# Kernel tuning notes

Measured on AMD Instinct MI355X. Metric: run time of the kernel, lower is better.

The kernel has to match this reference:

```python
import jax, jax.numpy as jnp
import numpy as np

N, E, C, L, NG = 50000, 600000, 128, 7, 512
EPS = 1e-7


def layer_norm(z, g, b):
    mu = z.mean(-1, keepdims=True)
    var = ((z - mu) ** 2).mean(-1, keepdims=True)
    return (z - mu) * jax.lax.rsqrt(var + 1e-5) * g + b


def setup_inputs() -> dict:
    key = jax.random.key(0)
    ks = jax.random.split(key, 16)
    inp = {
        'x': jax.random.randint(ks[0], (N, 9), 0, 64, dtype=jnp.int32),
        'edge_index': jax.random.randint(ks[1], (2, E), 0, N, dtype=jnp.int32),
        'edge_attr': jax.random.randint(ks[2], (E, 3), 0, 8, dtype=jnp.int32),
        'batch': jnp.sort(jax.random.randint(ks[3], (N,), 0, NG, dtype=jnp.int32)),
        'atom_emb': jax.random.normal(ks[4], (9, 64, C), jnp.float32) * 0.1,
        'bond_emb': jax.random.normal(ks[5], (3, 8, C), jnp.float32) * 0.1,
        'vn_emb': jnp.zeros((1, C), jnp.float32),
        'conv_W1': jax.random.normal(ks[6], (L, C, 2 * C), jnp.float32) / np.sqrt(C),
        'conv_b1': jnp.zeros((L, 2 * C), jnp.float32),
        'conv_g1': jnp.ones((L, 2 * C), jnp.float32),
        'conv_bb1': jnp.zeros((L, 2 * C), jnp.float32),
        'conv_W2': jax.random.normal(ks[7], (L, 2 * C, C), jnp.float32) / np.sqrt(2 * C),
        'conv_b2': jnp.zeros((L, C), jnp.float32),
        'norm_g': jnp.ones((L, C), jnp.float32),
        'norm_b': jnp.zeros((L, C), jnp.float32),
        'vn_W1': jax.random.normal(ks[8], (L - 1, C, C), jnp.float32) / np.sqrt(C),
        'vn_b1': jnp.zeros((L - 1, C), jnp.float32),
        'vn_g': jnp.ones((L - 1, C), jnp.float32),
        'vn_bb': jnp.zeros((L - 1, C), jnp.float32),
        'vn_W2': jax.random.normal(ks[9], (L - 1, C, C), jnp.float32) / np.sqrt(C),
        'vn_b2': jnp.zeros((L - 1, C), jnp.float32),
    }
    return inp


def reference(x, edge_index, edge_attr, batch, atom_emb, bond_emb, vn_emb,
              conv_W1, conv_b1, conv_g1, conv_bb1, conv_W2, conv_b2,
              norm_g, norm_b, vn_W1, vn_b1, vn_g, vn_bb, vn_W2, vn_b2):
    src, dst = edge_index[0], edge_index[1]

    # AtomEncoder: sum of per-feature embeddings -> [N, C]
    h = atom_emb[jnp.arange(9), x].sum(axis=1)
    # BondEncoder (conv_encode_edge=False) -> [E, C]
    edge_emb = bond_emb[jnp.arange(3), edge_attr].sum(axis=1)

    # virtual node embedding (one per graph)
    vn = jnp.broadcast_to(vn_emb[0], (NG, C))
    h = h + vn[batch]

    def gen_conv(l, hx):
        # GENConv: msg = relu(x_j + e) + eps; softmax aggregation (t=1); MLP(x+m)
        msg = jax.nn.relu(hx[src] + edge_emb) + EPS                      # [E, C]
        mx = jax.ops.segment_max(msg, dst, num_segments=N)               # [N, C]
        e = jnp.exp(msg - mx[dst])
        den = jax.ops.segment_sum(e, dst, num_segments=N)
        m = jax.ops.segment_sum(msg * (e / (den[dst] + 1e-16)), dst, num_segments=N)
        z = hx + m
        z = jax.nn.relu(layer_norm(z @ conv_W1[l] + conv_b1[l], conv_g1[l], conv_bb1[l]))
        return z @ conv_W2[l] + conv_b2[l]

    # res+ block: Conv -> [Norm -> ReLU -> (VN update) -> Conv + res]*
    h = gen_conv(0, h)
    for l in range(1, L):
        h2 = jax.nn.relu(layer_norm(h, norm_g[l - 1], norm_b[l - 1]))
        vtmp = jax.ops.segment_sum(h2, batch, num_segments=NG) + vn
        v = jax.nn.relu(layer_norm(vtmp @ vn_W1[l - 1] + vn_b1[l - 1], vn_g[l - 1], vn_bb[l - 1]))
        vn = v @ vn_W2[l - 1] + vn_b2[l - 1]
        h2 = h2 + vn[batch]
        h = gen_conv(l, h2) + h
    h = layer_norm(h, norm_g[L - 1], norm_b[L - 1])

    # global_add_pool -> [NG, C]
    return jax.ops.segment_sum(h, batch, num_segments=NG)
```

## Files before the change

kernel.cpp:

```cpp
#include <hip/hip_runtime.h>
#include <hip/hip_bf16.h>
#include <stdint.h>

#define N_NODES 50000
#define N_EDGES 600000
#define CH 128
#define NLAYERS 7
#define NGRAPHS 512

typedef __hip_bfloat16 bf16;
using bf16x8 = __attribute__((ext_vector_type(8))) __bf16;
using f32x4  = __attribute__((ext_vector_type(4))) float;
using u32x4  = __attribute__((ext_vector_type(4))) uint32_t;

static __device__ __forceinline__ float b2f(bf16 v){ return __bfloat162float(v); }

static __device__ __forceinline__ void bar_lds(){
  asm volatile("s_waitcnt lgkmcnt(0)" ::: "memory");
  __builtin_amdgcn_sched_barrier(0);
  __builtin_amdgcn_s_barrier();
}

__global__ void k_detect(const uint32_t* __restrict__ g, int* __restrict__ flag){
  if (threadIdx.x == 0 && blockIdx.x == 0) flag[0] = (g[0] == 0x3F803F80u) ? 1 : 0;
}

struct Segs { const void* src[12]; float* dst[12]; int n[12]; };

__global__ void k_cvt_all(const int* __restrict__ flag, Segs S){
  int f = flag[0];
  int seg = blockIdx.y;
  int n = S.n[seg];
  const void* src = S.src[seg];
  float* dst = S.dst[seg];
  for (int i = blockIdx.x*blockDim.x + threadIdx.x; i < n; i += gridDim.x*blockDim.x)
    dst[i] = f ? b2f(((const bf16*)src)[i]) : ((const float*)src)[i];
}

__global__ void k_transpose_all(const int* __restrict__ flag,
    const void* W1, const void* W2, const void* vW1, const void* vW2,
    bf16* W1p, bf16* W2T, bf16* vW1p, bf16* vW2T){
  int f = flag[0];
  const int T0 = NLAYERS*128*256, T1 = NLAYERS*256*128;
  const int T2 = (NLAYERS-1)*128*128;
  int total = T0+T1+2*T2;
  for (int i = blockIdx.x*blockDim.x + threadIdx.x; i < total; i += gridDim.x*blockDim.x){
    float v;
    if (i < T0){
      int idx = i; int l = idx/(128*256); int rem = idx - l*128*256; int k = rem >> 8; int n = rem & 255;
      v = f ? b2f(((const bf16*)W1)[idx]) : ((const float*)W1)[idx];
      W1p[(size_t)l*256*128 + n*128 + (k ^ ((n&7)<<3))] = __float2bfloat16(v);
    } else if (i < T0+T1){
      int idx = i-T0; int l = idx/(256*128); int rem = idx - l*256*128; int k = rem >> 7; int n = rem & 127;
      v = f ? b2f(((const bf16*)W2)[idx]) : ((const float*)W2)[idx];
      W2T[(size_t)l*128*256 + n*256 + k] = __float2bfloat16(v);
    } else if (i < T0+T1+T2){
      int idx = i-T0-T1; int l = idx/(128*128); int rem = idx - l*128*128; int k = rem >> 7; int n = rem & 127;
      v = f ? b2f(((const bf16*)vW1)[idx]) : ((const float*)vW1)[idx];
      vW1p[(size_t)l*128*128 + n*128 + (k ^ ((n&7)<<3))] = __float2bfloat16(v);
    } else {
      int idx = i-T0-T1-T2; int l = idx/(128*128); int rem = idx - l*128*128; int k = rem >> 7; int n = rem & 127;
      v = f ? b2f(((const bf16*)vW2)[idx]) : ((const float*)vW2)[idx];
      vW2T[(size_t)l*128*128 + n*128 + k] = __float2bfloat16(v);
    }
  }
}

__global__ void k_bondC(const int* __restrict__ flag, const void* __restrict__ bond,
                        float* __restrict__ bondC){
  int f = flag[0];
  int i = blockIdx.x*blockDim.x + threadIdx.x;
  if (i >= 512*128) return;
  int idx = i >> 7, c = i & 127;
  int a0 = idx & 7, a1 = (idx>>3) & 7, a2 = (idx>>6) & 7;
  auto g = [&](int e)->float{ return f ? b2f(((const bf16*)bond)[e]) : ((const float*)bond)[e]; };
  bondC[i] = g((0*8+a0)*128 + c) + g((1*8+a1)*128 + c) + g((2*8+a2)*128 + c);
}

__global__ void k_zero_i32(int* p, int n){
  for (int i = blockIdx.x*blockDim.x + threadIdx.x; i < n; i += gridDim.x*blockDim.x) p[i] = 0;
}

__global__ void k_hist(const int* __restrict__ keys, int* __restrict__ counts, int n){
  for (int i = blockIdx.x*blockDim.x + threadIdx.x; i < n; i += gridDim.x*blockDim.x)
    atomicAdd(&counts[keys[i]], 1);
}

__global__ __launch_bounds__(256) void k_scanA(const int* __restrict__ in, int* __restrict__ out,
                                               int* __restrict__ bsums, int n){
  __shared__ int lds[256];
  int t = threadIdx.x;
  int base = blockIdx.x * 1024;
  int v[4]; int s = 0;
  #pragma unroll
  for (int i=0;i<4;i++){ int idx = base + t*4 + i; int x = (idx<n)? in[idx] : 0; v[i]=x; s+=x; }
  lds[t] = s; __syncthreads();
  for (int off=1; off<256; off<<=1){
    int x = (t>=off)? lds[t-off] : 0;
    __syncthreads();
    lds[t] += x;
    __syncthreads();
  }
  int p = lds[t] - s;
  #pragma unroll
  for (int i=0;i<4;i++){ int idx = base + t*4 + i; if (idx<n) out[idx] = p; p += v[i]; }
  if (t==255) bsums[blockIdx.x] = lds[255];
}

__global__ __launch_bounds__(256) void k_scanB(int* bsums, int nblk){
  __shared__ int lds[256];
  int t = threadIdx.x;
  int v = (t<nblk)? bsums[t] : 0;
  lds[t] = v; __syncthreads();
  for (int off=1; off<256; off<<=1){
    int x = (t>=off)? lds[t-off] : 0;
    __syncthreads();
    lds[t] += x;
    __syncthreads();
  }
  if (t<nblk) bsums[t] = lds[t] - v;
}

__global__ void k_scanC(int* out, const int* bsums, int n){
  for (int i = blockIdx.x*blockDim.x + threadIdx.x; i < n; i += gridDim.x*blockDim.x)
    out[i] += bsums[i >> 10];
}

__global__ void k_scatter(const int* __restrict__ ei, const int* __restrict__ ea,
                          const int* __restrict__ row_ptr, int* __restrict__ fill,
                          uint32_t* __restrict__ csr){
  for (int e = blockIdx.x*blockDim.x + threadIdx.x; e < N_EDGES; e += gridDim.x*blockDim.x){
    int src = ei[e];
    int dst = ei[N_EDGES + e];
    int pos = row_ptr[dst] + atomicAdd(&fill[dst], 1);
    uint32_t a0 = (uint32_t)ea[e*3+0], a1 = (uint32_t)ea[e*3+1], a2 = (uint32_t)ea[e*3+2];
    csr[pos] = (uint32_t)src | ((a0 | (a1<<3) | (a2<<6)) << 16);
  }
}

__global__ void k_gptr(const int* __restrict__ batch, int* __restrict__ gptr){
  int i = blockIdx.x*blockDim.x + threadIdx.x;
  if (i >= N_NODES) return;
  int b = batch[i];
  if (i == 0){ for (int g=0; g<=b; ++g) gptr[g] = 0; }
  else { int bp = batch[i-1]; for (int g=bp+1; g<=b; ++g) gptr[g] = i; }
  if (i == N_NODES-1){ for (int g=b+1; g<=NGRAPHS; ++g) gptr[g] = N_NODES; }
}

__global__ __launch_bounds__(128) void k_atom_encode(const int* __restrict__ x,
    const float* __restrict__ atom_emb, const float* __restrict__ vn_emb,
    uint32_t* __restrict__ hxb){
  int n = blockIdx.x; int c = threadIdx.x;
  float s = vn_emb[c];
  #pragma unroll
  for (int f=0; f<9; ++f){
    int xv = x[n*9+f];
    s += atom_emb[(f*64 + xv)*CH + c];
  }
  float o = __shfl_xor(s, 1);
  if ((c & 1) == 0){
    __hip_bfloat162 p; p.x = __float2bfloat16(s); p.y = __float2bfloat16(o);
    hxb[n*64 + (c>>1)] = *reinterpret_cast<uint32_t*>(&p);
  }
}

__global__ void k_vn_init(const float* __restrict__ vn_emb, float* __restrict__ vn){
  for (int i = blockIdx.x*blockDim.x + threadIdx.x; i < NGRAPHS*CH; i += gridDim.x*blockDim.x)
    vn[i] = vn_emb[i & (CH-1)];
}

__global__ __launch_bounds__(64) void k_aggregate(const uint32_t* __restrict__ hxb,
     const uint32_t* __restrict__ csr, const int* __restrict__ row_ptr,
     const float* __restrict__ bondC, uint32_t* __restrict__ z){
  int n = blockIdx.x; int t = threadIdx.x;
  int s0 = row_ptr[n], s1 = row_ptr[n+1];
  float sa=0.f, sb=0.f, wa=0.f, wb=0.f;
  int i = s0;
  for (; i+4 <= s1; i += 4){
    uint32_t u0=csr[i], u1=csr[i+1], u2=csr[i+2], u3=csr[i+3];
    uint32_t h0 = hxb[(size_t)(u0 & 0xFFFFu)*64 + t];
    uint32_t h1 = hxb[(size_t)(u1 & 0xFFFFu)*64 + t];
    uint32_t h2 = hxb[(size_t)(u2 & 0xFFFFu)*64 + t];
    uint32_t h3 = hxb[(size_t)(u3 & 0xFFFFu)*64 + t];
    float2 c0 = *reinterpret_cast<const float2*>(bondC + (size_t)(u0 >> 16)*128 + 2*t);
    float2 c1 = *reinterpret_cast<const float2*>(bondC + (size_t)(u1 >> 16)*128 + 2*t);
    float2 c2 = *reinterpret_cast<const float2*>(bondC + (size_t)(u2 >> 16)*128 + 2*t);
    float2 c3 = *reinterpret_cast<const float2*>(bondC + (size_t)(u3 >> 16)*128 + 2*t);
    #define EDGE(hp, bc) { \
      float va = __uint_as_float(hp << 16) + bc.x; \
      float vb = __uint_as_float(hp & 0xFFFF0000u) + bc.y; \
      va = fmaxf(va, 0.f) + 1e-7f; vb = fmaxf(vb, 0.f) + 1e-7f; \
      float pa = __expf(va - 10.f), pb = __expf(vb - 10.f); \
      sa += pa; wa += pa*va; sb += pb; wb += pb*vb; }
    EDGE(h0, c0) EDGE(h1, c1) EDGE(h2, c2) EDGE(h3, c3)
  }
  for (; i < s1; ++i){
    uint32_t u = csr[i];
    uint32_t hp = hxb[(size_t)(u & 0xFFFFu)*64 + t];
    float2 bc = *reinterpret_cast<const float2*>(bondC + (size_t)(u >> 16)*128 + 2*t);
    EDGE(hp, bc)
    #undef EDGE
  }
  uint32_t own = hxb[(size_t)n*64 + t];
  float za = __uint_as_float(own << 16)         + wa/(sa + 1e-16f);
  float zb = __uint_as_float(own & 0xFFFF0000u) + wb/(sb + 1e-16f);
  __hip_bfloat162 p; p.x = __float2bfloat16(za); p.y = __float2bfloat16(zb);
  z[(size_t)n*64 + (t ^ ((n&7)<<2))] = *reinterpret_cast<uint32_t*>(&p);
}

template<int K, int N1, int N2, bool VNIN>
__global__ __launch_bounds__(512, 2) void k_mlp7(const bf16* __restrict__ A,
    const float* __restrict__ Af32,
    const bf16* __restrict__ W1s,
    const float* __restrict__ b1, const float* __restrict__ g1, const float* __restrict__ bb1,
    const bf16* __restrict__ W2T,
    const float* __restrict__ b2,
    const float* __restrict__ lng, const float* __restrict__ lnb,
    const float* __restrict__ residual, float* __restrict__ out,
    float* __restrict__ hxout, int relu2, int M, int NT)
{
  constexpr int KK1 = K/32;
  constexpr int WC  = N1/4;
  constexpr int JC  = WC/16;
  constexpr int KK2 = N1/32;
  __shared__ __align__(16) bf16 W1L[N1*K];
  __shared__ __align__(16) bf16 AL[2][64*K];
  __shared__ __align__(16) bf16 zt[64*N1];
  __shared__ float lnp[64][4][2];
  __shared__ float lnv[64][2];

  const int tid = threadIdx.x;
  const int wid = tid >> 6, lane = tid & 63;
  const int wr = wid >> 2, wc = wid & 3;
  const int rlo = lane & 15, hi = lane >> 4, khi = hi*8;

  {
    constexpr int NC_ = (N1*K*2)/1024/8;
    #pragma unroll
    for (int c=0;c<NC_;++c){
      int cc = c*8 + wid;
      __builtin_amdgcn_global_load_lds((const uint32_t*)((const char*)W1s + cc*1024 + lane*16),
                                       (uint32_t*)((char*)W1L + cc*1024), 16, 0, 0);
    }
  }

  float b1v[JC], gv[JC], bbv[JC];
  #pragma unroll
  for (int jc=0;jc<JC;++jc){
    int col = wc*WC + jc*16 + rlo;
    b1v[jc] = b1[col]; gv[jc] = g1[col]; bbv[jc] = bb1[col];
  }
  float bv2[2] = { b2[wc*32 + rlo], b2[wc*32 + 16 + rlo] };
  float lngv[2] = {0.f,0.f}, lnbv[2] = {0.f,0.f};
  if (hxout){
    lngv[0] = lng[wc*32 + rlo];      lnbv[0] = lnb[wc*32 + rlo];
    lngv[1] = lng[wc*32 + 16 + rlo]; lnbv[1] = lnb[wc*32 + 16 + rlo];
  }
  u32x4 b2raw[2][KK2];
  #pragma unroll
  for (int ct=0;ct<2;++ct){
    const bf16* wp = W2T + (size_t)(wc*32 + ct*16 + rlo)*N1 + khi;
    #pragma unroll
    for (int kk=0;kk<KK2;++kk){
      b2raw[ct][kk] = *reinterpret_cast<const u32x4*>(wp + kk*32);
      asm volatile("" : "+v"(b2raw[ct][kk]));
    }
  }

  auto stageA = [&](int nb, int tile){
    if constexpr (!VNIN){
      const char* src = (const char*)A + (size_t)tile*(64*K*2);
      constexpr int NCA = (64*K*2)/1024/8;
      #pragma unroll
      for (int c=0;c<NCA;++c){
        int cc = c*8 + wid;
        __builtin_amdgcn_global_load_lds((const uint32_t*)(src + cc*1024 + lane*16),
                                         (uint32_t*)((char*)&AL[nb][0] + cc*1024), 16, 0, 0);
      }
    } else {
      int base = tile*64;
      #pragma unroll
      for (int e=0;e<(64*K/4)/512;++e){
        int idx = tid + e*512;
        int row = idx >> 5;
        int k4  = (idx & 31)*4;
        float4 v = *reinterpret_cast<const float4*>(Af32 + (size_t)(base+row)*K + k4);
        int s = (row&7)<<3;
        bf16* d = &AL[nb][row*K + (k4 ^ s)];
        d[0]=__float2bfloat16(v.x); d[1]=__float2bfloat16(v.y);
        d[2]=__float2bfloat16(v.z); d[3]=__float2bfloat16(v.w);
      }
    }
  };

  int t = blockIdx.x, buf = 0;
  stageA(0, t);
  __syncthreads();

  while (true){
    int tn = t + (int)gridDim.x;

    f32x4 acc1[2][JC];
    #pragma unroll
    for (int rt=0;rt<2;++rt)
      #pragma unroll
      for (int jc=0;jc<JC;++jc) acc1[rt][jc] = {0.f,0.f,0.f,0.f};
    #pragma unroll
    for (int kk=0;kk<KK1;++kk){
      bf16x8 af[2], bw[JC];
      #pragma unroll
      for (int rt=0;rt<2;++rt){
        int lr = wr*32 + rt*16 + rlo;
        af[rt] = *reinterpret_cast<const bf16x8*>(&AL[buf][lr*K + ((kk*32 + khi) ^ ((lr&7)<<3))]);
      }
      #pragma unroll
      for (int jc=0;jc<JC;++jc){
        int n = wc*WC + jc*16 + rlo;
        bw[jc] = *reinterpret_cast<const bf16x8*>(&W1L[n*K + ((kk*32 + khi) ^ ((n&7)<<3))]);
      }
      #pragma unroll
      for (int rt=0;rt<2;++rt)
        #pragma unroll
        for (int jc=0;jc<JC;++jc)
          acc1[rt][jc] = __builtin_amdgcn_mfma_f32_16x16x32_bf16(af[rt], bw[jc], acc1[rt][jc], 0,0,0);
    }

    if (tn < NT) stageA(buf^1, tn);
    float resv[2][2][4];
    if (residual){
      #pragma unroll
      for (int rt=0;rt<2;++rt)
        #pragma unroll
        for (int r=0;r<4;++r){
          int grow = t*64 + wr*32 + rt*16 + hi*4 + r; if (grow >= M) grow = M-1;
          #pragma unroll
          for (int ct=0;ct<2;++ct)
            resv[rt][ct][r] = residual[(size_t)grow*N2 + wc*32 + ct*16 + rlo];
        }
    }
    __builtin_amdgcn_sched_barrier(0);

    float p[2][4], q[2][4];
    #pragma unroll
    for (int rt=0;rt<2;++rt)
      #pragma unroll
      for (int r=0;r<4;++r){ p[rt][r]=0.f; q[rt][r]=0.f; }
    #pragma unroll
    for (int jc=0;jc<JC;++jc)
      #pragma unroll
      for (int rt=0;rt<2;++rt)
        #pragma unroll
        for (int r=0;r<4;++r){
          float v = acc1[rt][jc][r] + b1v[jc]; acc1[rt][jc][r] = v;
          p[rt][r] += v; q[rt][r] += v*v;
        }
    #pragma unroll
    for (int rt=0;rt<2;++rt)
      #pragma unroll
      for (int r=0;r<4;++r){
        float pv = p[rt][r], qv = q[rt][r];
        #pragma unroll
        for (int off=1; off<16; off<<=1){ pv += __shfl_xor(pv, off); qv += __shfl_xor(qv, off); }
        if (rlo == 0){
          int row = wr*32 + rt*16 + hi*4 + r;
          lnp[row][wc][0] = pv; lnp[row][wc][1] = qv;
        }
      }
    bar_lds();
    if (tid < 64){
      float P=0.f, Q=0.f;
      #pragma unroll
      for (int w=0;w<4;++w){ P += lnp[tid][w][0]; Q += lnp[tid][w][1]; }
      float mu = P*(1.f/N1);
      lnv[tid][0] = mu;
      lnv[tid][1] = rsqrtf(Q*(1.f/N1) - mu*mu + 1e-5f);
    }
    bar_lds();

    #pragma unroll
    for (int rt=0;rt<2;++rt)
      #pragma unroll
      for (int r=0;r<4;++r){
        int row = wr*32 + rt*16 + hi*4 + r;
        float mu = lnv[row][0], rs = lnv[row][1];
        #pragma unroll
        for (int jc=0;jc<JC;++jc){
          int col = wc*WC + jc*16 + rlo;
          float y = (acc1[rt][jc][r]-mu)*rs*gv[jc] + bbv[jc];
          zt[row*N1 + (col ^ ((row&7)<<3))] = __float2bfloat16(fmaxf(y, 0.f));
        }
      }
    bar_lds();

    f32x4 acc2[2][2];
    #pragma unroll
    for (int rt=0;rt<2;++rt)
      #pragma unroll
      for (int ct=0;ct<2;++ct) acc2[rt][ct] = {0.f,0.f,0.f,0.f};
    #pragma unroll
    for (int kk=0;kk<KK2;++kk){
      bf16x8 a2[2];
      #pragma unroll
      for (int rt=0;rt<2;++rt){
        int row = wr*32 + rt*16 + rlo;
        a2[rt] = *reinterpret_cast<const bf16x8*>(&zt[row*N1 + ((kk*32 + khi) ^ ((row&7)<<3))]);
      }
      #pragma unroll
      for (int rt=0;rt<2;++rt)
        #pragma unroll
        for (int ct=0;ct<2;++ct){
          bf16x8 bb;
          __builtin_memcpy(&bb, &b2raw[ct][kk], 16);
          acc2[rt][ct] = __builtin_amdgcn_mfma_f32_16x16x32_bf16(a2[rt], bb, acc2[rt][ct], 0,0,0);
        }
    }

    float vmat[2][2][4];
    #pragma unroll
    for (int rt=0;rt<2;++rt)
      #pragma unroll
      for (int ct=0;ct<2;++ct)
        #pragma unroll
        for (int r=0;r<4;++r){
          float v = acc2[rt][ct][r] + bv2[ct];
          if (residual) v += resv[rt][ct][r];
          vmat[rt][ct][r] = v;
          int grow = t*64 + wr*32 + rt*16 + hi*4 + r;
          if (grow < M) out[(size_t)grow*N2 + wc*32 + ct*16 + rlo] = v;
        }

    if (hxout){
      #pragma unroll
      for (int rt=0;rt<2;++rt)
        #pragma unroll
        for (int r=0;r<4;++r){
          float pv = vmat[rt][0][r] + vmat[rt][1][r];
          float qv = vmat[rt][0][r]*vmat[rt][0][r] + vmat[rt][1][r]*vmat[rt][1][r];
          #pragma unroll
          for (int off=1; off<16; off<<=1){ pv += __shfl_xor(pv, off); qv += __shfl_xor(qv, off); }
          if (rlo == 0){
            int row = wr*32 + rt*16 + hi*4 + r;
            lnp[row][wc][0] = pv; lnp[row][wc][1] = qv;
          }
        }
      bar_lds();
      if (tid < 64){
        float P=0.f, Q=0.f;
        #pragma unroll
        for (int w=0;w<4;++w){ P += lnp[tid][w][0]; Q += lnp[tid][w][1]; }
        float mu = P*(1.f/N2);
        lnv[tid][0] = mu;
        lnv[tid][1] = rsqrtf(Q*(1.f/N2) - mu*mu + 1e-5f);
      }
      bar_lds();
      #pragma unroll
      for (int rt=0;rt<2;++rt)
        #pragma unroll
        for (int r=0;r<4;++r){
          int row = wr*32 + rt*16 + hi*4 + r;
          float mu = lnv[row][0], rs = lnv[row][1];
          int grow = t*64 + row;
          if (grow < M){
            #pragma unroll
            for (int ct=0;ct<2;++ct){
              float y = (vmat[rt][ct][r]-mu)*rs*lngv[ct] + lnbv[ct];
              if (relu2) y = fmaxf(y, 0.f);
              hxout[(size_t)grow*N2 + wc*32 + ct*16 + rlo] = y;
            }
          }
        }
    }

    if (tn >= NT) break;
    t = tn; buf ^= 1;
    __syncthreads();
  }
}

__global__ void k_vncopy(const float* __restrict__ vn, float* __restrict__ vnacc){
  int i = blockIdx.x*blockDim.x + threadIdx.x;
  if (i < NGRAPHS*CH) vnacc[i] = vn[i];
}

#define SEGC 128
__global__ __launch_bounds__(128) void k_segsum2(const float* __restrict__ hx,
    const int* __restrict__ batch, float* __restrict__ vnacc){
  int c = threadIdx.x;
  int n0 = blockIdx.x*SEGC;
  int n1 = n0 + SEGC; if (n1 > N_NODES) n1 = N_NODES;
  if (n0 >= N_NODES) return;
  int cur = batch[n0];
  float s = 0.f;
  for (int n = n0; n < n1; ++n){
    int b = batch[n];
    if (b != cur){ atomicAdd(&vnacc[cur*CH + c], s); s = 0.f; cur = b; }
    s += hx[(size_t)n*CH + c];
  }
  atomicAdd(&vnacc[cur*CH + c], s);
}

__global__ void k_add_vn(const float* __restrict__ hx, const float* __restrict__ vn,
                         const int* __restrict__ batch, uint32_t* __restrict__ hxb){
  for (int i = blockIdx.x*blockDim.x + threadIdx.x; i < N_NODES*64; i += gridDim.x*blockDim.x){
    int n = i >> 6; int t = i & 63;
    float2 hv = *reinterpret_cast<const float2*>(hx + (size_t)n*CH + 2*t);
    float2 vv = *reinterpret_cast<const float2*>(vn + (size_t)batch[n]*CH + 2*t);
    __hip_bfloat162 p; p.x = __float2bfloat16(hv.x+vv.x); p.y = __float2bfloat16(hv.y+vv.y);
    hxb[i] = *reinterpret_cast<uint32_t*>(&p);
  }
}

__global__ __launch_bounds__(128) void k_pool(const float* __restrict__ hx,
    const int* __restrict__ gptr, const int* __restrict__ flag, void* __restrict__ out){
  int g = blockIdx.x; int c = threadIdx.x;
  float s = 0.f;
  for (int n = gptr[g]; n < gptr[g+1]; ++n) s += hx[(size_t)n*CH + c];
  if (flag[0]) ((bf16*)out)[g*CH+c] = __float2bfloat16(s);
  else         ((float*)out)[g*CH+c] = s;
}

extern "C" void kernel_launch(void* const* d_in, const int* in_sizes, int n_in,
                              void* d_out, int out_size, void* d_ws, size_t ws_size,
                              hipStream_t stream)
{
  const int*  x     = (const int*) d_in[0];
  const int*  ei    = (const int*) d_in[1];
  const int*  ea    = (const int*) d_in[2];
  const int*  batch = (const int*) d_in[3];
  const void* atom_emb = d_in[4];
  const void* bond_emb = d_in[5];
  const void* vn_emb   = d_in[6];
  const void* conv_W1  = d_in[7];
  const void* conv_b1  = d_in[8];
  const void* conv_g1  = d_in[9];
  const void* conv_bb1 = d_in[10];
  const void* conv_W2  = d_in[11];
  const void* conv_b2  = d_in[12];
  const void* norm_g   = d_in[13];
  const void* norm_b   = d_in[14];
  const void* vn_W1    = d_in[15];
  const void* vn_b1    = d_in[16];
  const void* vn_g     = d_in[17];
  const void* vn_bb    = d_in[18];
  const void* vn_W2    = d_in[19];
  const void* vn_b2    = d_in[20];

  char* wsb = (char*)d_ws;
  size_t off = 0;
  auto alloc = [&](size_t bytes)->char*{ char* p = wsb + off; off += (bytes + 255) & ~(size_t)255; return p; };
  const int ZROWS = 50048;
  float*    h     = (float*)   alloc(sizeof(float)*N_NODES*CH);
  float*    hx    = (float*)   alloc(sizeof(float)*N_NODES*CH);
  uint32_t* hxb   = (uint32_t*)alloc(sizeof(uint32_t)*N_NODES*64);
  uint32_t* z     = (uint32_t*)alloc(sizeof(uint32_t)*ZROWS*64);
  float*    vn    = (float*)   alloc(sizeof(float)*NGRAPHS*CH);
  float*    vnacc = (float*)   alloc(sizeof(float)*NGRAPHS*CH);
  bf16*     W1Tp  = (bf16*)    alloc(sizeof(bf16)*NLAYERS*256*128);
  bf16*     W2T   = (bf16*)    alloc(sizeof(bf16)*NLAYERS*128*256);
  bf16*     vW1Tp = (bf16*)    alloc(sizeof(bf16)*(NLAYERS-1)*128*128);
  bf16*     vW2T  = (bf16*)    alloc(sizeof(bf16)*(NLAYERS-1)*128*128);
  int* row_ptr = (int*)alloc(sizeof(int)*(N_NODES+1));
  int* counts  = (int*)alloc(sizeof(int)*(N_NODES+1));
  uint32_t* csr = (uint32_t*)alloc(sizeof(uint32_t)*N_EDGES);
  int* gptr    = (int*)alloc(sizeof(int)*(NGRAPHS+1));
  int* bsums   = (int*)alloc(sizeof(int)*256);
  int* flag    = (int*)alloc(sizeof(int)*64);
  float* atomF = (float*)alloc(sizeof(float)*9*64*CH);
  float* bondC = (float*)alloc(sizeof(float)*512*CH);
  float* vnEF  = (float*)alloc(sizeof(float)*CH);
  float* b1F   = (float*)alloc(sizeof(float)*NLAYERS*2*CH);
  float* g1F   = (float*)alloc(sizeof(float)*NLAYERS*2*CH);
  float* bb1F  = (float*)alloc(sizeof(float)*NLAYERS*2*CH);
  float* b2F   = (float*)alloc(sizeof(float)*NLAYERS*CH);
  float* ngF   = (float*)alloc(sizeof(float)*NLAYERS*CH);
  float* nbF   = (float*)alloc(sizeof(float)*NLAYERS*CH);
  float* vb1F  = (float*)alloc(sizeof(float)*(NLAYERS-1)*CH);
  float* vgF   = (float*)alloc(sizeof(float)*(NLAYERS-1)*CH);
  float* vbbF  = (float*)alloc(sizeof(float)*(NLAYERS-1)*CH);
  float* vb2F  = (float*)alloc(sizeof(float)*(NLAYERS-1)*CH);

  k_detect<<<1, 64, 0, stream>>>((const uint32_t*)norm_g, flag);
  Segs S;
  int si = 0;
  auto seg = [&](const void* s_, float* d_, int n_){ S.src[si]=s_; S.dst[si]=d_; S.n[si]=n_; ++si; };
  seg(atom_emb, atomF, 9*64*CH);
  seg(vn_emb,   vnEF,  CH);
  seg(conv_b1,  b1F,  NLAYERS*2*CH);
  seg(conv_g1,  g1F,  NLAYERS*2*CH);
  seg(conv_bb1, bb1F, NLAYERS*2*CH);
  seg(conv_b2,  b2F,  NLAYERS*CH);
  seg(norm_g,   ngF,  NLAYERS*CH);
  seg(norm_b,   nbF,  NLAYERS*CH);
  seg(vn_b1,    vb1F, (NLAYERS-1)*CH);
  seg(vn_g,     vgF,  (NLAYERS-1)*CH);
  seg(vn_bb,    vbbF, (NLAYERS-1)*CH);
  seg(vn_b2,    vb2F, (NLAYERS-1)*CH);
  k_cvt_all<<<dim3(72, 12), 256, 0, stream>>>(flag, S);
  k_transpose_all<<<640, 256, 0, stream>>>(flag, conv_W1, conv_W2, vn_W1, vn_W2,
                                           W1Tp, W2T, vW1Tp, vW2T);
  k_bondC<<<256, 256, 0, stream>>>(flag, bond_emb, bondC);

  k_zero_i32<<<64, 256, 0, stream>>>(counts, N_NODES+1);
  k_hist<<<512, 256, 0, stream>>>(ei + N_EDGES, counts, N_EDGES);
  int nblkE = (N_NODES+1 + 1023)/1024;
  k_scanA<<<nblkE, 256, 0, stream>>>(counts, row_ptr, bsums, N_NODES+1);
  k_scanB<<<1, 256, 0, stream>>>(bsums, nblkE);
  k_scanC<<<64, 256, 0, stream>>>(row_ptr, bsums, N_NODES+1);
  k_zero_i32<<<64, 256, 0, stream>>>(counts, N_NODES+1);
  k_scatter<<<512, 256, 0, stream>>>(ei, ea, row_ptr, counts, csr);
  k_gptr<<<(N_NODES+255)/256, 256, 0, stream>>>(batch, gptr);

  k_atom_encode<<<N_NODES, 128, 0, stream>>>(x, atomF, vnEF, hxb);
  k_vn_init<<<64, 256, 0, stream>>>(vnEF, vn);

  const int NT_CONV = (N_NODES + 63)/64;
  const int NT_VN   = NGRAPHS/64;

  for (int l = 0; l < NLAYERS; ++l){
    if (l > 0){
      k_vncopy<<<(NGRAPHS*CH+255)/256, 256, 0, stream>>>(vn, vnacc);
      k_segsum2<<<(N_NODES+SEGC-1)/SEGC, 128, 0, stream>>>(hx, batch, vnacc);
      k_mlp7<128,128,128,true><<<NT_VN, 512, 0, stream>>>(nullptr, vnacc,
          vW1Tp + (size_t)(l-1)*128*128, vb1F + (l-1)*CH, vgF + (l-1)*CH, vbbF + (l-1)*CH,
          vW2T + (size_t)(l-1)*128*128, vb2F + (l-1)*CH,
          nullptr, nullptr, nullptr, vn, nullptr, 0, NGRAPHS, NT_VN);
      k_add_vn<<<1024, 256, 0, stream>>>(hx, vn, batch, hxb);
    }
    k_aggregate<<<N_NODES, 64, 0, stream>>>(hxb, csr, row_ptr, bondC, z);
    k_mlp7<128,256,128,false><<<256, 512, 0, stream>>>((const bf16*)z, nullptr,
        W1Tp + (size_t)l*256*128, b1F + l*2*CH, g1F + l*2*CH, bb1F + l*2*CH,
        W2T + (size_t)l*128*256, b2F + l*CH,
        ngF + l*CH, nbF + l*CH,
        (l==0)? nullptr : h, h, hx, (l < NLAYERS-1) ? 1 : 0, N_NODES, NT_CONV);
  }
  k_pool<<<NGRAPHS, 128, 0, stream>>>(hx, gptr, flag, d_out);
}
```

Baseline: 965.8 us.

## Store residual, normalized activations and bond table in bf16; remap aggregate block order

Switches the residual stream h and the normalized activation hx from fp32 to bf16 storage. The MLP kernel gains a BF16IO template path, and segsum, add_vn and pool now read bf16. The bond combination table is also packed as bf16 pairs, and k_aggregate interleaves node indices across blocks in groups of eight. This halves memory traffic for the per-layer activation reads and writes, at the cost of accumulating the residual in bf16 across seven layers, which risks accuracy drift.

```diff
diff --git a/kernel.cpp b/kernel.cpp
--- a/kernel.cpp
+++ b/kernel.cpp
@@ -67,14 +67,18 @@
 }
 
 __global__ void k_bondC(const int* __restrict__ flag, const void* __restrict__ bond,
-                        float* __restrict__ bondC){
+                        uint32_t* __restrict__ bondC){
+  int i = blockIdx.x*blockDim.x + threadIdx.x;
+  if (i >= 512*64) return;
   int f = flag[0];
-  int i = blockIdx.x*blockDim.x + threadIdx.x;
-  if (i >= 512*128) return;
-  int idx = i >> 7, c = i & 127;
+  int idx = i >> 6, t = i & 63;
   int a0 = idx & 7, a1 = (idx>>3) & 7, a2 = (idx>>6) & 7;
   auto g = [&](int e)->float{ return f ? b2f(((const bf16*)bond)[e]) : ((const float*)bond)[e]; };
-  bondC[i] = g((0*8+a0)*128 + c) + g((1*8+a1)*128 + c) + g((2*8+a2)*128 + c);
+  int c0 = 2*t, c1 = 2*t+1;
+  float s0 = g((0*8+a0)*128 + c0) + g((1*8+a1)*128 + c0) + g((2*8+a2)*128 + c0);
+  float s1 = g((0*8+a0)*128 + c1) + g((1*8+a1)*128 + c1) + g((2*8+a2)*128 + c1);
+  __hip_bfloat162 p; p.x = __float2bfloat16(s0); p.y = __float2bfloat16(s1);
+  bondC[i] = *reinterpret_cast<uint32_t*>(&p);
 }
 
 __global__ void k_zero_i32(int* p, int n){
@@ -171,8 +175,9 @@
 
 __global__ __launch_bounds__(64) void k_aggregate(const uint32_t* __restrict__ hxb,
      const uint32_t* __restrict__ csr, const int* __restrict__ row_ptr,
-     const float* __restrict__ bondC, uint32_t* __restrict__ z){
-  int n = blockIdx.x; int t = threadIdx.x;
+     const uint32_t* __restrict__ bondC, uint32_t* __restrict__ z){
+  int n = (blockIdx.x & 7)*(N_NODES/8) + (blockIdx.x >> 3);
+  int t = threadIdx.x;
   int s0 = row_ptr[n], s1 = row_ptr[n+1];
   float sa=0.f, sb=0.f, wa=0.f, wb=0.f;
   int i = s0;
@@ -182,13 +187,13 @@
     uint32_t h1 = hxb[(size_t)(u1 & 0xFFFFu)*64 + t];
     uint32_t h2 = hxb[(size_t)(u2 & 0xFFFFu)*64 + t];
     uint32_t h3 = hxb[(size_t)(u3 & 0xFFFFu)*64 + t];
-    float2 c0 = *reinterpret_cast<const float2*>(bondC + (size_t)(u0 >> 16)*128 + 2*t);
-    float2 c1 = *reinterpret_cast<const float2*>(bondC + (size_t)(u1 >> 16)*128 + 2*t);
-    float2 c2 = *reinterpret_cast<const float2*>(bondC + (size_t)(u2 >> 16)*128 + 2*t);
-    float2 c3 = *reinterpret_cast<const float2*>(bondC + (size_t)(u3 >> 16)*128 + 2*t);
+    uint32_t c0 = bondC[(size_t)(u0 >> 16)*64 + t];
+    uint32_t c1 = bondC[(size_t)(u1 >> 16)*64 + t];
+    uint32_t c2 = bondC[(size_t)(u2 >> 16)*64 + t];
+    uint32_t c3 = bondC[(size_t)(u3 >> 16)*64 + t];
     #define EDGE(hp, bc) { \
-      float va = __uint_as_float(hp << 16) + bc.x; \
-      float vb = __uint_as_float(hp & 0xFFFF0000u) + bc.y; \
+      float va = __uint_as_float(hp << 16) + __uint_as_float(bc << 16); \
+      float vb = __uint_as_float(hp & 0xFFFF0000u) + __uint_as_float(bc & 0xFFFF0000u); \
       va = fmaxf(va, 0.f) + 1e-7f; vb = fmaxf(vb, 0.f) + 1e-7f; \
       float pa = __expf(va - 10.f), pb = __expf(vb - 10.f); \
       sa += pa; wa += pa*va; sb += pb; wb += pb*vb; }
@@ -197,7 +202,7 @@
   for (; i < s1; ++i){
     uint32_t u = csr[i];
     uint32_t hp = hxb[(size_t)(u & 0xFFFFu)*64 + t];
-    float2 bc = *reinterpret_cast<const float2*>(bondC + (size_t)(u >> 16)*128 + 2*t);
+    uint32_t bc = bondC[(size_t)(u >> 16)*64 + t];
     EDGE(hp, bc)
     #undef EDGE
   }
@@ -208,16 +213,16 @@
   z[(size_t)n*64 + (t ^ ((n&7)<<2))] = *reinterpret_cast<uint32_t*>(&p);
 }
 
-template<int K, int N1, int N2, bool VNIN>
-__global__ __launch_bounds__(512, 2) void k_mlp7(const bf16* __restrict__ A,
+template<int K, int N1, int N2, bool VNIN, bool BF16IO>
+__global__ __launch_bounds__(512, 2) void k_mlp12(const bf16* __restrict__ A,
     const float* __restrict__ Af32,
     const bf16* __restrict__ W1s,
     const float* __restrict__ b1, const float* __restrict__ g1, const float* __restrict__ bb1,
     const bf16* __restrict__ W2T,
     const float* __restrict__ b2,
     const float* __restrict__ lng, const float* __restrict__ lnb,
-    const float* __restrict__ residual, float* __restrict__ out,
-    float* __restrict__ hxout, int relu2, int M, int NT)
+    const void* __restrict__ residual, void* __restrict__ out,
+    bf16* __restrict__ hxn, int relu2, int M, int NT)
 {
   constexpr int KK1 = K/32;
   constexpr int WC  = N1/4;
@@ -252,7 +257,7 @@
   }
   float bv2[2] = { b2[wc*32 + rlo], b2[wc*32 + 16 + rlo] };
   float lngv[2] = {0.f,0.f}, lnbv[2] = {0.f,0.f};
-  if (hxout){
+  if (hxn){
     lngv[0] = lng[wc*32 + rlo];      lnbv[0] = lnb[wc*32 + rlo];
     lngv[1] = lng[wc*32 + 16 + rlo]; lnbv[1] = lnb[wc*32 + 16 + rlo];
   }
@@ -334,8 +339,11 @@
         for (int r=0;r<4;++r){
           int grow = t*64 + wr*32 + rt*16 + hi*4 + r; if (grow >= M) grow = M-1;
           #pragma unroll
-          for (int ct=0;ct<2;++ct)
-            resv[rt][ct][r] = residual[(size_t)grow*N2 + wc*32 + ct*16 + rlo];
+          for (int ct=0;ct<2;++ct){
+            size_t off = (size_t)grow*N2 + wc*32 + ct*16 + rlo;
+            resv[rt][ct][r] = BF16IO ? b2f(((const bf16*)residual)[off])
+                                     : ((const float*)residual)[off];
+          }
         }
     }
     __builtin_amdgcn_sched_barrier(0);
@@ -426,10 +434,14 @@
           if (residual) v += resv[rt][ct][r];
           vmat[rt][ct][r] = v;
           int grow = t*64 + wr*32 + rt*16 + hi*4 + r;
-          if (grow < M) out[(size_t)grow*N2 + wc*32 + ct*16 + rlo] = v;
-        }
-
-    if (hxout){
+          if (grow < M){
+            size_t off = (size_t)grow*N2 + wc*32 + ct*16 + rlo;
+            if (BF16IO) ((bf16*)out)[off] = __float2bfloat16(v);
+            else        ((float*)out)[off] = v;
+          }
+        }
+
+    if (hxn){
       #pragma unroll
       for (int rt=0;rt<2;++rt)
         #pragma unroll
@@ -465,7 +477,7 @@
             for (int ct=0;ct<2;++ct){
               float y = (vmat[rt][ct][r]-mu)*rs*lngv[ct] + lnbv[ct];
               if (relu2) y = fmaxf(y, 0.f);
-              hxout[(size_t)grow*N2 + wc*32 + ct*16 + rlo] = y;
+              hxn[(size_t)grow*N2 + wc*32 + ct*16 + rlo] = __float2bfloat16(y);
             }
           }
         }
@@ -483,7 +495,7 @@
 }
 
 #define SEGC 128
-__global__ __launch_bounds__(128) void k_segsum2(const float* __restrict__ hx,
+__global__ __launch_bounds__(128) void k_segsum2(const bf16* __restrict__ hxn,
     const int* __restrict__ batch, float* __restrict__ vnacc){
   int c = threadIdx.x;
   int n0 = blockIdx.x*SEGC;
@@ -494,27 +506,29 @@
   for (int n = n0; n < n1; ++n){
     int b = batch[n];
     if (b != cur){ atomicAdd(&vnacc[cur*CH + c], s); s = 0.f; cur = b; }
-    s += hx[(size_t)n*CH + c];
+    s += b2f(hxn[(size_t)n*CH + c]);
   }
   atomicAdd(&vnacc[cur*CH + c], s);
 }
 
-__global__ void k_add_vn(const float* __restrict__ hx, const float* __restrict__ vn,
+__global__ void k_add_vn(const uint32_t* __restrict__ hxn, const float* __restrict__ vn,
                          const int* __restrict__ batch, uint32_t* __restrict__ hxb){
   for (int i = blockIdx.x*blockDim.x + threadIdx.x; i < N_NODES*64; i += gridDim.x*blockDim.x){
     int n = i >> 6; int t = i & 63;
-    float2 hv = *reinterpret_cast<const float2*>(hx + (size_t)n*CH + 2*t);
+    uint32_t hp = hxn[i];
     float2 vv = *reinterpret_cast<const float2*>(vn + (size_t)batch[n]*CH + 2*t);
-    __hip_bfloat162 p; p.x = __float2bfloat16(hv.x+vv.x); p.y = __float2bfloat16(hv.y+vv.y);
+    float za = __uint_as_float(hp << 16)         + vv.x;
+    float zb = __uint_as_float(hp & 0xFFFF0000u) + vv.y;
+    __hip_bfloat162 p; p.x = __float2bfloat16(za); p.y = __float2bfloat16(zb);
     hxb[i] = *reinterpret_cast<uint32_t*>(&p);
   }
 }
 
-__global__ __launch_bounds__(128) void k_pool(const float* __restrict__ hx,
+__global__ __launch_bounds__(128) void k_pool(const bf16* __restrict__ hxn,
     const int* __restrict__ gptr, const int* __restrict__ flag, void* __restrict__ out){
   int g = blockIdx.x; int c = threadIdx.x;
   float s = 0.f;
-  for (int n = gptr[g]; n < gptr[g+1]; ++n) s += hx[(size_t)n*CH + c];
+  for (int n = gptr[g]; n < gptr[g+1]; ++n) s += b2f(hxn[(size_t)n*CH + c]);
   if (flag[0]) ((bf16*)out)[g*CH+c] = __float2bfloat16(s);
   else         ((float*)out)[g*CH+c] = s;
 }
@@ -549,8 +563,8 @@
   size_t off = 0;
   auto alloc = [&](size_t bytes)->char*{ char* p = wsb + off; off += (bytes + 255) & ~(size_t)255; return p; };
   const int ZROWS = 50048;
-  float*    h     = (float*)   alloc(sizeof(float)*N_NODES*CH);
-  float*    hx    = (float*)   alloc(sizeof(float)*N_NODES*CH);
+  uint32_t* hb    = (uint32_t*)alloc(sizeof(uint32_t)*ZROWS*64);
+  uint32_t* hxn   = (uint32_t*)alloc(sizeof(uint32_t)*ZROWS*64);
   uint32_t* hxb   = (uint32_t*)alloc(sizeof(uint32_t)*N_NODES*64);
   uint32_t* z     = (uint32_t*)alloc(sizeof(uint32_t)*ZROWS*64);
   float*    vn    = (float*)   alloc(sizeof(float)*NGRAPHS*CH);
@@ -566,7 +580,7 @@
   int* bsums   = (int*)alloc(sizeof(int)*256);
   int* flag    = (int*)alloc(sizeof(int)*64);
   float* atomF = (float*)alloc(sizeof(float)*9*64*CH);
-  float* bondC = (float*)alloc(sizeof(float)*512*CH);
+  uint32_t* bondC = (uint32_t*)alloc(sizeof(uint32_t)*512*64);
   float* vnEF  = (float*)alloc(sizeof(float)*CH);
   float* b1F   = (float*)alloc(sizeof(float)*NLAYERS*2*CH);
   float* g1F   = (float*)alloc(sizeof(float)*NLAYERS*2*CH);
@@ -598,7 +612,7 @@
   k_cvt_all<<<dim3(72, 12), 256, 0, stream>>>(flag, S);
   k_transpose_all<<<640, 256, 0, stream>>>(flag, conv_W1, conv_W2, vn_W1, vn_W2,
                                            W1Tp, W2T, vW1Tp, vW2T);
-  k_bondC<<<256, 256, 0, stream>>>(flag, bond_emb, bondC);
+  k_bondC<<<128, 256, 0, stream>>>(flag, bond_emb, bondC);
 
   k_zero_i32<<<64, 256, 0, stream>>>(counts, N_NODES+1);
   k_hist<<<512, 256, 0, stream>>>(ei + N_EDGES, counts, N_EDGES);
@@ -619,19 +633,20 @@
   for (int l = 0; l < NLAYERS; ++l){
     if (l > 0){
       k_vncopy<<<(NGRAPHS*CH+255)/256, 256, 0, stream>>>(vn, vnacc);
-      k_segsum2<<<(N_NODES+SEGC-1)/SEGC, 128, 0, stream>>>(hx, batch, vnacc);
-      k_mlp7<128,128,128,true><<<NT_VN, 512, 0, stream>>>(nullptr, vnacc,
+      k_segsum2<<<(N_NODES+SEGC-1)/SEGC, 128, 0, stream>>>((const bf16*)hxn, batch, vnacc);
+      k_mlp12<128,128,128,true,false><<<NT_VN, 512, 0, stream>>>(nullptr, vnacc,
           vW1Tp + (size_t)(l-1)*128*128, vb1F + (l-1)*CH, vgF + (l-1)*CH, vbbF + (l-1)*CH,
           vW2T + (size_t)(l-1)*128*128, vb2F + (l-1)*CH,
           nullptr, nullptr, nullptr, vn, nullptr, 0, NGRAPHS, NT_VN);
-      k_add_vn<<<1024, 256, 0, stream>>>(hx, vn, batch, hxb);
+      k_add_vn<<<1024, 256, 0, stream>>>(hxn, vn, batch, hxb);
     }
     k_aggregate<<<N_NODES, 64, 0, stream>>>(hxb, csr, row_ptr, bondC, z);
-    k_mlp7<128,256,128,false><<<256, 512, 0, stream>>>((const bf16*)z, nullptr,
+    k_mlp12<128,256,128,false,true><<<256, 512, 0, stream>>>((const bf16*)z, nullptr,
         W1Tp + (size_t)l*256*128, b1F + l*2*CH, g1F + l*2*CH, bb1F + l*2*CH,
         W2T + (size_t)l*128*256, b2F + l*CH,
         ngF + l*CH, nbF + l*CH,
-        (l==0)? nullptr : h, h, hx, (l < NLAYERS-1) ? 1 : 0, N_NODES, NT_CONV);
-  }
-  k_pool<<<NGRAPHS, 128, 0, stream>>>(hx, gptr, flag, d_out);
-}
+        (l==0)? nullptr : (const void*)hb, (void*)hb, (bf16*)hxn,
+        (l < NLAYERS-1) ? 1 : 0, N_NODES, NT_CONV);
+  }
+  k_pool<<<NGRAPHS, 128, 0, stream>>>((const bf16*)hxn, gptr, flag, d_out);
+}
```

Result: no change. 952.6 us (median of 3 runs) (-1.4%).
